# Kernel tuning notes

Measured on AMD Instinct MI355X. Metric: run time of the kernel, lower is better.

The kernel has to match this reference:

```python
import jax, jax.numpy as jnp
import numpy as np

NUM_LAYERS = 4
D_MODEL = 1024
N_HEAD = 8
HEAD_DIM = D_MODEL // N_HEAD
FFN_DIM = 4096
B, L = 8, 512
LN_EPS = 1e-5


def rel_pos_embed(seq_len, dim, init_size=1200, padding_idx=0):
    # RelativeSinusoidalPositionalEmbedding.get_embedding(init_size+1, dim, 0)
    num = init_size + 1  # 1201
    half = dim // 2
    inv = np.exp(np.arange(half, dtype=np.float64) * -(np.log(10000.0) / (half - 1)))
    pos = np.arange(-num // 2, num // 2, dtype=np.float64)[:, None] * inv[None, :]
    emb = np.concatenate([np.sin(pos), np.cos(pos)], axis=1)  # [num, dim]
    emb[padding_idx] = 0.0
    origin_shift = num // 2 + 1  # 601
    idx = np.arange(-seq_len, seq_len) + origin_shift  # [2L]
    return jnp.asarray(emb[idx], dtype=jnp.float32)  # [2L, dim]


def _shift(BD):
    # [b,h,L,2L] -> [b,h,L,L], selecting relative offsets k-q
    b, h, l, _ = BD.shape
    BD = jnp.concatenate([BD, jnp.zeros((b, h, l, 1), BD.dtype)], axis=-1)
    BD = BD.reshape(b, h, -1, l)[:, :, :-1].reshape(b, h, l, 2 * l)
    return BD[:, :, :, l:]


def _transpose_shift(E):
    # [b,h,L,2L] -> [b,h,L,L]
    b, h, l, _ = E.shape
    E = jnp.concatenate([E, jnp.zeros((b, h, l, 1), E.dtype)], axis=-1)
    E = E.reshape(b, h, 2 * l + 1, l)
    E = E[:, :, 2 * jnp.arange(l) + 1, :]  # [b,h,L,L]
    return jnp.swapaxes(E, -1, -2)


def layer_norm(x, g, b):
    mu = x.mean(-1, keepdims=True)
    var = ((x - mu) ** 2).mean(-1, keepdims=True)
    return (x - mu) / jnp.sqrt(var + LN_EPS) * g + b


def rel_attn(x, mask, qkv_w, r_r, r_w, pos):
    bsz, l, d = x.shape
    qkv = x @ qkv_w  # [b,L,3D]
    q, k, v = jnp.split(qkv, 3, axis=-1)
    to_heads = lambda t: t.reshape(bsz, l, N_HEAD, HEAD_DIM).transpose(0, 2, 1, 3)
    q, k, v = to_heads(q), to_heads(k), to_heads(v)  # [b,h,L,hd]
    rw_q = q + r_r[:, None]  # (original adds r_r_bias here)
    AC = jnp.einsum('bnqd,bnkd->bnqk', rw_q, k)
    D_ = jnp.einsum('nd,ld->nl', r_w, pos)[None, :, None]   # [1,h,1,2L]
    B_ = jnp.einsum('bnqd,ld->bnql', q, pos)                # [b,h,L,2L]
    E_ = jnp.einsum('bnqd,ld->bnql', k, pos)
    BDE = _shift(B_ + D_) + _transpose_shift(E_)
    attn = AC + BDE  # scale == 1 (scale=False)
    attn = jnp.where(mask[:, None, None, :] == 0, -jnp.inf, attn)
    attn = jax.nn.softmax(attn, axis=-1)
    out = jnp.einsum('bnqk,bnkd->bnqd', attn, v)
    return out.transpose(0, 2, 1, 3).reshape(bsz, l, d)


def setup_inputs() -> dict:
    key = jax.random.key(0)
    ks = jax.random.split(key, 12)
    Ln = NUM_LAYERS
    s = 0.02
    return {
        'x': jax.random.normal(ks[0], (B, L, D_MODEL), jnp.float32),
        'mask': jnp.ones((B, L), jnp.int32),
        'qkv_w': jax.random.normal(ks[1], (Ln, D_MODEL, 3 * D_MODEL), jnp.float32) * s,
        'r_r_bias': jax.random.normal(ks[2], (Ln, N_HEAD, HEAD_DIM), jnp.float32) * s,
        'r_w_bias': jax.random.normal(ks[3], (Ln, N_HEAD, HEAD_DIM), jnp.float32) * s,
        'ln1_g': jnp.ones((Ln, D_MODEL), jnp.float32),
        'ln1_b': jnp.zeros((Ln, D_MODEL), jnp.float32),
        'ln2_g': jnp.ones((Ln, D_MODEL), jnp.float32),
        'ln2_b': jnp.zeros((Ln, D_MODEL), jnp.float32),
        'w1': jax.random.normal(ks[4], (Ln, D_MODEL, FFN_DIM), jnp.float32) * s,
        'b1': jnp.zeros((Ln, FFN_DIM), jnp.float32),
        'w2': jax.random.normal(ks[5], (Ln, FFN_DIM, D_MODEL), jnp.float32) * s,
        'b2': jnp.zeros((Ln, D_MODEL), jnp.float32),
    }


def reference(x, mask, qkv_w, r_r_bias, r_w_bias, ln1_g, ln1_b, ln2_g, ln2_b, w1, b1, w2, b2):
    pos = rel_pos_embed(x.shape[1], HEAD_DIM)  # [2L, hd], buffer (detached)
    for i in range(NUM_LAYERS):  # after_norm=True (post-LN)
        a = rel_attn(x, mask, qkv_w[i], r_r_bias[i], r_w_bias[i], pos)
        x = layer_norm(x + a, ln1_g[i], ln1_b[i])
        h = jax.nn.relu(x @ w1[i] + b1[i]) @ w2[i] + b2[i]
        x = layer_norm(x + h, ln2_g[i], ln2_b[i])
    return x
```

## Files before the change

kernel.cpp:

```cpp
#include <hip/hip_runtime.h>

#define SEQ 512
#define DM 1024
#define NH 8
#define HD 128
#define FFN 4096
#define NL 4
#define NB 8

typedef __attribute__((ext_vector_type(8))) _Float16 half8v;
typedef __attribute__((ext_vector_type(8))) unsigned short ushort8v;
typedef __attribute__((ext_vector_type(4))) float float4v;

__device__ __forceinline__ unsigned short f2h(float f) {
  _Float16 h = (_Float16)f;
  return *(unsigned short*)&h;
}
__device__ __forceinline__ float h2f(unsigned short u) {
  _Float16 h = *(_Float16*)&u;
  return (float)h;
}

__global__ void prep_kernel(float* __restrict__ sc,
                            const float* __restrict__ in, float* __restrict__ xout,
                            unsigned short* __restrict__ xh) {
  if (blockIdx.x < 128) {
    int idx = blockIdx.x * 256 + threadIdx.x;
    int q = idx >> 6, c = idx & 63;
    double a = exp(-(double)c * (9.210340371976184 / 63.0));
    double p = (double)q * a;
    sc[q * 128 + c] = (float)sin(p);
    sc[q * 128 + 64 + c] = (float)cos(p);
  } else {
    int i = (blockIdx.x - 128) * 256 + threadIdx.x;
    float4 v = ((const float4*)in)[i];
    ((float4*)xout)[i] = v;
    ushort4 u;
    u.x = f2h(v.x); u.y = f2h(v.y); u.z = f2h(v.z); u.w = f2h(v.w);
    ((ushort4*)xh)[i] = u;
  }
}

__global__ __launch_bounds__(256) void transpose_cvt3(
    const float* __restrict__ qw, const float* __restrict__ w1,
    const float* __restrict__ w2,
    unsigned short* __restrict__ wqt, unsigned short* __restrict__ w1t,
    unsigned short* __restrict__ w2t)
{
  __shared__ float t[32][33];
  int id = blockIdx.x;
  const float* in;
  unsigned short* out;
  int K, N, loc;
  if (id < 3072)      { in = qw; out = wqt; K = 1024; N = 3072; loc = id; }
  else if (id < 7168) { in = w1; out = w1t; K = 1024; N = 4096; loc = id - 3072; }
  else                { in = w2; out = w2t; K = 4096; N = 1024; loc = id - 7168; }
  int nx = N >> 5;
  int n0 = (loc % nx) * 32, k0 = (loc / nx) * 32;
  int c = threadIdx.x & 31, r = threadIdx.x >> 5;
#pragma unroll
  for (int i = 0; i < 32; i += 8)
    t[r + i][c] = in[(long long)(k0 + r + i) * N + n0 + c];
  __syncthreads();
#pragma unroll
  for (int i = 0; i < 32; i += 8)
    out[(long long)(n0 + r + i) * K + k0 + c] = f2h(t[c][r + i]);
}

template<int R, int T>
__device__ __forceinline__ void stage_tile(
    const unsigned short* __restrict__ g, long long ld, int k0,
    unsigned short* lds, int tid) {
#pragma unroll
  for (int i = 0; i < R * 64 / 8 / T; i++) {
    int p = i * T + tid;
    int row = p >> 3, cs = p & 7;
    int c = cs ^ (row & 7);
    const unsigned short* src = g + (long long)row * ld + k0 + c * 8;
    __builtin_amdgcn_global_load_lds(
        (const __attribute__((address_space(1))) void*)src,
        (__attribute__((address_space(3))) void*)(lds + p * 8),
        16, 0, 0);
  }
}

__device__ __forceinline__ void load_stage128(
    const unsigned short* __restrict__ g, long long ld, int k0, int tid, ushort8v* v) {
#pragma unroll
  for (int i = 0; i < 2; i++) {
    int p = i * 512 + tid;
    int row = p >> 3, cs = p & 7;
    int c = cs ^ (row & 7);
    v[i] = *(const ushort8v*)(g + (long long)row * ld + k0 + c * 8);
  }
}
__device__ __forceinline__ void write_stage128(
    unsigned short* St, int tid, const ushort8v* v) {
#pragma unroll
  for (int i = 0; i < 2; i++)
    *(ushort8v*)(St + (i * 512 + tid) * 8) = v[i];
}

template<int BIAS, int RELU, int OUTH>
__global__ __launch_bounds__(512, 2) void gemm256(
    const unsigned short* __restrict__ A, int lda, long long sAz,
    const unsigned short* __restrict__ Bt, int ldb, long long sBz,
    const float* __restrict__ bias,
    void* __restrict__ Cv, int ldc, long long sCz,
    int K) {
  __shared__ __align__(16) unsigned short As[2][256 * 64];
  __shared__ __align__(16) unsigned short Bs[2][256 * 64];
  const int tid = threadIdx.x, lane = tid & 63, w = tid >> 6;
  const int wm = w >> 2, wn = w & 3;
  const int l15 = lane & 15, l4 = lane >> 4;
  const int gx = gridDim.x, gy = gridDim.y;
  int nwg = gx * gy * gridDim.z;
  int lin = (blockIdx.z * gy + blockIdx.y) * gx + blockIdx.x;
  int swz = (lin & 7) * (nwg >> 3) + (lin >> 3);
  int bx = swz % gx;
  int t2 = swz / gx;
  int by = t2 % gy;
  int z  = t2 / gy;
  const unsigned short* Ag = A + (long long)z * sAz + (long long)by * 256 * lda;
  const unsigned short* Bg = Bt + (long long)z * sBz + (long long)bx * 256 * ldb;

  float4v acc[8][4] = {};
  const int nt = K >> 6;
  stage_tile<256, 512>(Ag, lda, 0, As[0], tid);
  stage_tile<256, 512>(Bg, ldb, 0, Bs[0], tid);
  int cur = 0;
  for (int t = 0; t < nt; t++) {
    if (t + 1 < nt) {
      stage_tile<256, 512>(Ag, lda, (t + 1) << 6, As[cur ^ 1], tid);
      stage_tile<256, 512>(Bg, ldb, (t + 1) << 6, Bs[cur ^ 1], tid);
      asm volatile("s_waitcnt vmcnt(8)" ::: "memory");
    } else {
      asm volatile("s_waitcnt vmcnt(0)" ::: "memory");
    }
    asm volatile("s_barrier" ::: "memory");
#pragma unroll
    for (int ks = 0; ks < 2; ks++) {
      half8v af[8], bf[4];
#pragma unroll
      for (int m = 0; m < 8; m++) {
        int row = wm * 128 + m * 16 + l15;
        int cs = (ks * 4 + l4) ^ (row & 7);
        af[m] = *(const half8v*)&As[cur][row * 64 + cs * 8];
      }
#pragma unroll
      for (int n = 0; n < 4; n++) {
        int row = wn * 64 + n * 16 + l15;
        int cs = (ks * 4 + l4) ^ (row & 7);
        bf[n] = *(const half8v*)&Bs[cur][row * 64 + cs * 8];
      }
#pragma unroll
      for (int m = 0; m < 8; m++)
#pragma unroll
        for (int n = 0; n < 4; n++)
          acc[m][n] = __builtin_amdgcn_mfma_f32_16x16x32_f16(af[m], bf[n], acc[m][n], 0, 0, 0);
    }
    asm volatile("s_barrier" ::: "memory");
    cur ^= 1;
  }
#pragma unroll
  for (int n = 0; n < 4; n++) {
    int ccol = bx * 256 + wn * 64 + n * 16 + l15;
    float bv = BIAS ? bias[ccol] : 0.f;
#pragma unroll
    for (int m = 0; m < 8; m++) {
      int crow0 = by * 256 + wm * 128 + m * 16 + l4 * 4;
#pragma unroll
      for (int j = 0; j < 4; j++) {
        float v = acc[m][n][j] + bv;
        if (RELU) v = fmaxf(v, 0.f);
        long long off = (long long)z * sCz + (long long)(crow0 + j) * ldc + ccol;
        if (OUTH) ((unsigned short*)Cv)[off] = f2h(v);
        else      ((float*)Cv)[off] = v;
      }
    }
  }
}

__global__ __launch_bounds__(256) void build_attn(
    const unsigned short* __restrict__ qkv_h,
    const float* __restrict__ rr, const float* __restrict__ rw,
    const float* __restrict__ sc,
    unsigned short* __restrict__ Ahat, unsigned short* __restrict__ Bhat,
    unsigned short* __restrict__ Vt)
{
  const int z = blockIdx.y, b = z >> 3, h = z & 7;
  if (blockIdx.x < 256) {
    const int r = threadIdx.x >> 7, lane = threadIdx.x & 127;
    const int q = blockIdx.x * 2 + r;
    __shared__ float Qf[2][128], Kf[2][128], SC[2][128];
    const unsigned short* row = qkv_h + ((long long)(b * SEQ + q)) * 3072 + h * HD;
    float qv = h2f(row[lane]);
    float kv = h2f(row[DM + lane]);
    Qf[r][lane] = qv + rw[h * HD + lane];
    Kf[r][lane] = kv;
    SC[r][lane] = sc[q * 128 + lane];
    __syncthreads();
    unsigned short* Arow = Ahat + ((long long)z * SEQ + q) * 384;
    unsigned short* Brow = Bhat + ((long long)z * SEQ + q) * 384;
    Arow[lane] = f2h(qv + rr[h * HD + lane]);
    Brow[lane] = f2h(kv);
    if (lane < 64) {
      float S = SC[r][lane], C = SC[r][64 + lane];
      Arow[128 + lane] = f2h(Qf[r][lane] * C + Qf[r][64 + lane] * S);
      Arow[256 + lane] = f2h(S);
      Brow[128 + lane] = f2h(S);
      Brow[256 + lane] = f2h(Kf[r][lane] * C + Kf[r][64 + lane] * S);
    } else {
      int c = lane - 64;
      float S = SC[r][c], C = SC[r][lane];
      Arow[192 + c] = f2h(Qf[r][lane] * C - Qf[r][c] * S);
      Arow[320 + c] = f2h(C);
      Brow[192 + c] = f2h(C);
      Brow[320 + c] = f2h(Kf[r][lane] * C - Kf[r][c] * S);
    }
  } else {
    __shared__ unsigned short t[32][33];
    int tile = blockIdx.x - 256;
    const int d0 = (tile & 3) * 32, j0 = (tile >> 2) * 32;
    const int c = threadIdx.x & 31, r = threadIdx.x >> 5;
#pragma unroll
    for (int i = 0; i < 32; i += 8)
      t[r + i][c] = qkv_h[((long long)(b * SEQ + j0 + r + i)) * 3072 + 2 * DM + h * HD + d0 + c];
    __syncthreads();
#pragma unroll
    for (int i = 0; i < 32; i += 8)
      Vt[(long long)z * HD * SEQ + (long long)(d0 + r + i) * SEQ + j0 + c] = t[c][r + i];
  }
}

__global__ __launch_bounds__(512, 4) void attn_fused(
    const unsigned short* __restrict__ Ahat,
    const unsigned short* __restrict__ Bhat,
    const unsigned short* __restrict__ Vt,
    const int* __restrict__ mask,
    unsigned short* __restrict__ out)
{
  __shared__ __align__(16) unsigned short S[64 * 512];
  __shared__ __align__(16) unsigned short St[128 * 64];
  const int tid = threadIdx.x, lane = tid & 63, w = tid >> 6;
  const int wr = w >> 1, wc = w & 1;
  const int l15 = lane & 15, l4 = lane >> 4;
  int lin = blockIdx.z * gridDim.x + blockIdx.x;
  int nwg = gridDim.x * gridDim.z;
  int swz = (lin & 7) * (nwg >> 3) + (lin >> 3);
  int qt = swz % gridDim.x, z = swz / gridDim.x;
  const int b = z >> 3, h = z & 7;
  const int q0 = qt * 64;

  half8v qf[12];
  {
    const unsigned short* Ar = Ahat + ((long long)z * SEQ + q0 + wr * 16 + l15) * 384;
#pragma unroll
    for (int k = 0; k < 12; k++)
      qf[k] = *(const half8v*)&Ar[k * 32 + l4 * 8];
  }

  ushort8v stg[2];
  load_stage128(Bhat + ((long long)z * SEQ) * 384, 384, 0, tid, stg);
#pragma unroll
  for (int jt = 0; jt < 4; jt++) {
    float4v acc[4] = {};
#pragma unroll
    for (int k6 = 0; k6 < 6; k6++) {
      __builtin_amdgcn_s_barrier();
      write_stage128(St, tid, stg);
      int ns = jt * 6 + k6 + 1;
      if (ns < 24) {
        const unsigned short* Bg = Bhat + ((long long)z * SEQ + (ns / 6) * 128) * 384;
        load_stage128(Bg, 384, (ns % 6) * 64, tid, stg);
      }
      asm volatile("s_waitcnt lgkmcnt(0)" ::: "memory");
      __builtin_amdgcn_s_barrier();
      __builtin_amdgcn_s_setprio(1);
#pragma unroll
      for (int kk = 0; kk < 2; kk++) {
        int kidx = k6 * 2 + kk;
#pragma unroll
        for (int n = 0; n < 4; n++) {
          int row = wc * 64 + n * 16 + l15;
          int cs = (kk * 4 + l4) ^ (row & 7);
          half8v bf = *(const half8v*)&St[row * 64 + cs * 8];
          acc[n] = __builtin_amdgcn_mfma_f32_16x16x32_f16(qf[kidx], bf, acc[n], 0, 0, 0);
        }
      }
      __builtin_amdgcn_s_setprio(0);
    }
#pragma unroll
    for (int n = 0; n < 4; n++) {
      int col = jt * 128 + wc * 64 + n * 16 + l15;
#pragma unroll
      for (int j = 0; j < 4; j++) {
        int row = wr * 16 + l4 * 4 + j;
        int byte = (row * 512 + col) * 2;
        byte ^= (row & 7) << 4;
        *(unsigned short*)((char*)S + byte) = f2h(acc[n][j]);
      }
    }
  }

  const unsigned short* Vg = Vt + (long long)z * HD * SEQ;
  load_stage128(Vg, 512, 0, tid, stg);

  asm volatile("s_waitcnt lgkmcnt(0)" ::: "memory");
  __builtin_amdgcn_s_barrier();

  float* bias = (float*)St;
  float* Linv = (float*)St + 512;
  if (tid < 128) {
    int4 mk = ((const int4*)(mask + (size_t)b * SEQ))[tid];
    float4 bv;
    bv.x = mk.x ? 0.f : -1e30f;
    bv.y = mk.y ? 0.f : -1e30f;
    bv.z = mk.z ? 0.f : -1e30f;
    bv.w = mk.w ? 0.f : -1e30f;
    ((float4*)bias)[tid] = bv;
  }
  asm volatile("s_waitcnt lgkmcnt(0)" ::: "memory");
  __builtin_amdgcn_s_barrier();
  {
    const int row = tid >> 3;
    const int c8 = tid & 7;
    float mx = -1e30f;
#pragma unroll
    for (int i = 0; i < 8; i++) {
      int col = i * 64 + c8 * 8;
      int byte = (row * 512 + col) * 2;
      byte ^= (row & 7) << 4;
      ushort8v u = *(const ushort8v*)((const char*)S + byte);
      const float* bp = bias + col;
#pragma unroll
      for (int e = 0; e < 8; e++)
        mx = fmaxf(mx, h2f(u[e]) + bp[e]);
    }
    mx = fmaxf(mx, __shfl_xor(mx, 1));
    mx = fmaxf(mx, __shfl_xor(mx, 2));
    mx = fmaxf(mx, __shfl_xor(mx, 4));
    float sum = 0.f;
#pragma unroll
    for (int i = 0; i < 8; i++) {
      int col = i * 64 + c8 * 8;
      int byte = (row * 512 + col) * 2;
      byte ^= (row & 7) << 4;
      ushort8v u = *(const ushort8v*)((const char*)S + byte);
      const float* bp = bias + col;
#pragma unroll
      for (int e = 0; e < 8; e++) {
        float ev = __expf(h2f(u[e]) + bp[e] - mx);
        sum += ev;
        u[e] = f2h(ev);
      }
      *(ushort8v*)((char*)S + byte) = u;
    }
    sum += __shfl_xor(sum, 1);
    sum += __shfl_xor(sum, 2);
    sum += __shfl_xor(sum, 4);
    if (c8 == 0) Linv[row] = 1.f / sum;
  }
  asm volatile("s_waitcnt lgkmcnt(0)" ::: "memory");
  __builtin_amdgcn_s_barrier();
  float rs[4];
#pragma unroll
  for (int j = 0; j < 4; j++) rs[j] = Linv[wr * 16 + l4 * 4 + j];
  asm volatile("s_waitcnt lgkmcnt(0)" ::: "memory");

  float4v oacc[4] = {};
#pragma unroll
  for (int k8 = 0; k8 < 8; k8++) {
    __builtin_amdgcn_s_barrier();
    write_stage128(St, tid, stg);
    if (k8 + 1 < 8) load_stage128(Vg, 512, (k8 + 1) * 64, tid, stg);
    asm volatile("s_waitcnt lgkmcnt(0)" ::: "memory");
    __builtin_amdgcn_s_barrier();
    __builtin_amdgcn_s_setprio(1);
#pragma unroll
    for (int kk = 0; kk < 2; kk++) {
      int prow = wr * 16 + l15;
      int pb = (prow * 512 + k8 * 64 + kk * 32 + l4 * 8) * 2;
      pb ^= (prow & 7) << 4;
      half8v af = *(const half8v*)((const char*)S + pb);
#pragma unroll
      for (int n = 0; n < 4; n++) {
        int row = wc * 64 + n * 16 + l15;
        int cs = (kk * 4 + l4) ^ (row & 7);
        half8v bf = *(const half8v*)&St[row * 64 + cs * 8];
        oacc[n] = __builtin_amdgcn_mfma_f32_16x16x32_f16(af, bf, oacc[n], 0, 0, 0);
      }
    }
    __builtin_amdgcn_s_setprio(0);
  }
#pragma unroll
  for (int j = 0; j < 4; j++) {
    int row = q0 + wr * 16 + l4 * 4 + j;
#pragma unroll
    for (int n = 0; n < 4; n++) {
      int col = h * HD + wc * 64 + n * 16 + l15;
      out[((long long)(b * SEQ + row)) * DM + col] = f2h(oacc[n][j] * rs[j]);
    }
  }
}

__global__ __launch_bounds__(256) void add_ln_cvt(
    float* __restrict__ x, const unsigned short* __restrict__ a,
    const float* __restrict__ g, const float* __restrict__ bt,
    unsigned short* __restrict__ xh)
{
  const int row = blockIdx.x, tid = threadIdx.x;
  float4* xp = (float4*)(x + (size_t)row * DM);
  const ushort4 av = ((const ushort4*)(a + (size_t)row * DM))[tid];
  float4 xv = xp[tid];
  float4 s = make_float4(xv.x + h2f(av.x), xv.y + h2f(av.y),
                         xv.z + h2f(av.z), xv.w + h2f(av.w));
  __shared__ float red[4];
  float sum = s.x + s.y + s.z + s.w;
  for (int o = 32; o; o >>= 1) sum += __shfl_down(sum, o);
  if ((tid & 63) == 0) red[tid >> 6] = sum;
  __syncthreads();
  float mu = (red[0] + red[1] + red[2] + red[3]) * (1.f / DM);
  float dx = s.x - mu, dy = s.y - mu, dz = s.z - mu, dw = s.w - mu;
  float sq = dx * dx + dy * dy + dz * dz + dw * dw;
  for (int o = 32; o; o >>= 1) sq += __shfl_down(sq, o);
  __syncthreads();
  if ((tid & 63) == 0) red[tid >> 6] = sq;
  __syncthreads();
  float var = (red[0] + red[1] + red[2] + red[3]) * (1.f / DM);
  float rstd = rsqrtf(var + 1e-5f);
  const float4 gv = ((const float4*)g)[tid];
  const float4 bv = ((const float4*)bt)[tid];
  float4 o4 = make_float4(dx * rstd * gv.x + bv.x, dy * rstd * gv.y + bv.y,
                          dz * rstd * gv.z + bv.z, dw * rstd * gv.w + bv.w);
  xp[tid] = o4;
  ushort4 u;
  u.x = f2h(o4.x); u.y = f2h(o4.y); u.z = f2h(o4.z); u.w = f2h(o4.w);
  ((ushort4*)(xh + (size_t)row * DM))[tid] = u;
}

__global__ __launch_bounds__(256) void add_ln_cvt4(
    float* __restrict__ x, const unsigned short* __restrict__ p, long long pstride,
    const float* __restrict__ bias,
    const float* __restrict__ g, const float* __restrict__ bt,
    unsigned short* __restrict__ xh)
{
  const int row = blockIdx.x, tid = threadIdx.x;
  float4* xp = (float4*)(x + (size_t)row * DM);
  const float4 bb = ((const float4*)bias)[tid];
  float4 xv = xp[tid];
  float4 s = make_float4(xv.x + bb.x, xv.y + bb.y, xv.z + bb.z, xv.w + bb.w);
#pragma unroll
  for (int zz = 0; zz < 4; zz++) {
    const ushort4 a = ((const ushort4*)(p + zz * pstride + (size_t)row * DM))[tid];
    s.x += h2f(a.x); s.y += h2f(a.y); s.z += h2f(a.z); s.w += h2f(a.w);
  }
  __shared__ float red[4];
  float sum = s.x + s.y + s.z + s.w;
  for (int o = 32; o; o >>= 1) sum += __shfl_down(sum, o);
  if ((tid & 63) == 0) red[tid >> 6] = sum;
  __syncthreads();
  float mu = (red[0] + red[1] + red[2] + red[3]) * (1.f / DM);
  float dx = s.x - mu, dy = s.y - mu, dz = s.z - mu, dw = s.w - mu;
  float sq = dx * dx + dy * dy + dz * dz + dw * dw;
  for (int o = 32; o; o >>= 1) sq += __shfl_down(sq, o);
  __syncthreads();
  if ((tid & 63) == 0) red[tid >> 6] = sq;
  __syncthreads();
  float var = (red[0] + red[1] + red[2] + red[3]) * (1.f / DM);
  float rstd = rsqrtf(var + 1e-5f);
  const float4 gv = ((const float4*)g)[tid];
  const float4 bv = ((const float4*)bt)[tid];
  float4 o4 = make_float4(dx * rstd * gv.x + bv.x, dy * rstd * gv.y + bv.y,
                          dz * rstd * gv.z + bv.z, dw * rstd * gv.w + bv.w);
  xp[tid] = o4;
  ushort4 u;
  u.x = f2h(o4.x); u.y = f2h(o4.y); u.z = f2h(o4.z); u.w = f2h(o4.w);
  ((ushort4*)(xh + (size_t)row * DM))[tid] = u;
}

extern "C" void kernel_launch(void* const* d_in, const int* in_sizes, int n_in,
                              void* d_out, int out_size, void* d_ws, size_t ws_size,
                              hipStream_t stream)
{
  const float* x_in = (const float*)d_in[0];
  const int*   mask = (const int*)d_in[1];
  const float* qkv_w = (const float*)d_in[2];
  const float* r_r  = (const float*)d_in[3];
  const float* r_w  = (const float*)d_in[4];
  const float* ln1g = (const float*)d_in[5];
  const float* ln1b = (const float*)d_in[6];
  const float* ln2g = (const float*)d_in[7];
  const float* ln2b = (const float*)d_in[8];
  const float* w1   = (const float*)d_in[9];
  const float* b1   = (const float*)d_in[10];
  const float* w2   = (const float*)d_in[11];
  const float* b2   = (const float*)d_in[12];
  float* x = (float*)d_out;
  char* ws = (char*)d_ws;

  const int ROWS = NB * SEQ;

  const size_t sc_off   = 0;
  const size_t xh_off   = 0x40000;
  const size_t wqt_off  = xh_off + (size_t)ROWS * DM * 2;
  const size_t w1t_off  = wqt_off + (size_t)3 * DM * DM * 2;
  const size_t w2t_off  = w1t_off + (size_t)FFN * DM * 2;
  const size_t a16_off  = w2t_off + (size_t)FFN * DM * 2;
  const size_t qkvh_off = a16_off + (size_t)ROWS * DM * 2;
  const size_t e_off    = qkvh_off + (size_t)ROWS * 3 * DM * 2;

  const size_t ab_bytes = (size_t)64 * SEQ * 384 * 2;
  const size_t hb_bytes = (size_t)ROWS * FFN * 2;
  const size_t part_off = e_off + hb_bytes;

  float* sc     = (float*)(ws + sc_off);
  unsigned short* xh = (unsigned short*)(ws + xh_off);
  unsigned short* wqt = (unsigned short*)(ws + wqt_off);
  unsigned short* w1t = (unsigned short*)(ws + w1t_off);
  unsigned short* w2t = (unsigned short*)(ws + w2t_off);
  unsigned short* a16 = (unsigned short*)(ws + a16_off);
  unsigned short* qkvh = (unsigned short*)(ws + qkvh_off);
  unsigned short* Ahat = (unsigned short*)(ws + e_off);
  unsigned short* Bhat = (unsigned short*)(ws + e_off + ab_bytes);
  unsigned short* Vt   = (unsigned short*)(ws + e_off + 2 * ab_bytes);
  unsigned short* hb = (unsigned short*)(ws + e_off);
  unsigned short* part = (unsigned short*)(ws + part_off);

  prep_kernel<<<dim3(128 + ROWS * DM / 4 / 256), 256, 0, stream>>>(sc, x_in, x, xh);

  for (int L = 0; L < NL; L++) {
    transpose_cvt3<<<dim3(11264), 256, 0, stream>>>(
        qkv_w + (size_t)L * DM * 3 * DM, w1 + (size_t)L * DM * FFN,
        w2 + (size_t)L * FFN * DM, wqt, w1t, w2t);

    gemm256<0,0,1><<<dim3(3 * DM / 256, ROWS / 256, 1), 512, 0, stream>>>(
        xh, DM, 0, wqt, DM, 0, nullptr, qkvh, 3 * DM, 0, DM);

    build_attn<<<dim3(256 + 64, 64), 256, 0, stream>>>(
        qkvh, r_r + (size_t)L * NH * HD, r_w + (size_t)L * NH * HD, sc, Ahat, Bhat, Vt);
    attn_fused<<<dim3(SEQ / 64, 1, 64), 512, 0, stream>>>(Ahat, Bhat, Vt, mask, a16);

    add_ln_cvt<<<dim3(ROWS), 256, 0, stream>>>(x, a16, ln1g + (size_t)L * DM, ln1b + (size_t)L * DM, xh);

    gemm256<1,1,1><<<dim3(FFN / 256, ROWS / 256, 1), 512, 0, stream>>>(
        xh, DM, 0, w1t, DM, 0, b1 + (size_t)L * FFN, hb, FFN, 0, DM);

    gemm256<0,0,1><<<dim3(DM / 256, ROWS / 256, 4), 512, 0, stream>>>(
        hb, FFN, 1024, w2t, FFN, 1024, nullptr,
        part, DM, (long long)ROWS * DM, 1024);

    add_ln_cvt4<<<dim3(ROWS), 256, 0, stream>>>(
        x, part, (long long)ROWS * DM, b2 + (size_t)L * DM,
        ln2g + (size_t)L * DM, ln2b + (size_t)L * DM, xh);
  }
}
```

Before: 838.4 us.

## Split GEMM K-tile into half-stages with finer-grained interleaved prefetch and setprio

Restructures the 256x256 GEMM main loop so each 64-wide K tile is split into two 32-wide LDS sub-buffers. Global-to-LDS loads are issued in small chunks between four MFMA phases, with barriers between phases and s_setprio raised around the MFMA blocks, in the style of ping-pong scheduling. The goal is to overlap memory traffic with matrix math more evenly and to cut LDS bank conflicts through a new XOR swizzle. The cost is many more barriers per iteration and delicate vmcnt accounting that could stall or race if any count is wrong.

```diff
diff --git a/kernel.cpp b/kernel.cpp
--- a/kernel.cpp
+++ b/kernel.cpp
@@ -84,6 +84,22 @@
   }
 }
 
+__device__ __forceinline__ void stageK(
+    const unsigned short* __restrict__ g, long long ld, int k0,
+    unsigned short* lds, int tid) {
+#pragma unroll
+  for (int i = 0; i < 2; i++) {
+    int p = i * 512 + tid;
+    int row = p >> 2, cs = p & 3;
+    int c = cs ^ ((row >> 1) & 3);
+    const unsigned short* src = g + (long long)row * ld + k0 + c * 8;
+    __builtin_amdgcn_global_load_lds(
+        (const __attribute__((address_space(1))) void*)src,
+        (__attribute__((address_space(3))) void*)(lds + p * 8),
+        16, 0, 0);
+  }
+}
+
 __device__ __forceinline__ void load_stage128(
     const unsigned short* __restrict__ g, long long ld, int k0, int tid, ushort8v* v) {
 #pragma unroll
@@ -108,8 +124,8 @@
     const float* __restrict__ bias,
     void* __restrict__ Cv, int ldc, long long sCz,
     int K) {
-  __shared__ __align__(16) unsigned short As[2][256 * 64];
-  __shared__ __align__(16) unsigned short Bs[2][256 * 64];
+  __shared__ __align__(16) unsigned short As[2][2][256 * 32];
+  __shared__ __align__(16) unsigned short Bs[2][2][256 * 32];
   const int tid = threadIdx.x, lane = tid & 63, w = tid >> 6;
   const int wm = w >> 2, wn = w & 3;
   const int l15 = lane & 15, l4 = lane >> 4;
@@ -126,41 +142,91 @@
 
   float4v acc[8][4] = {};
   const int nt = K >> 6;
-  stage_tile<256, 512>(Ag, lda, 0, As[0], tid);
-  stage_tile<256, 512>(Bg, ldb, 0, Bs[0], tid);
-  int cur = 0;
+  stageK(Ag, lda, 0,  As[0][0], tid); stageK(Bg, ldb, 0,  Bs[0][0], tid);
+  stageK(Ag, lda, 32, As[0][1], tid); stageK(Bg, ldb, 32, Bs[0][1], tid);
+  stageK(Ag, lda, 64, As[1][0], tid); stageK(Bg, ldb, 64, Bs[1][0], tid);
+  stageK(Ag, lda, 96, As[1][1], tid);
+  asm volatile("s_waitcnt vmcnt(6)" ::: "memory");
+  asm volatile("s_barrier" ::: "memory");
+
+  half8v af[8], bf[4];
   for (int t = 0; t < nt; t++) {
-    if (t + 1 < nt) {
-      stage_tile<256, 512>(Ag, lda, (t + 1) << 6, As[cur ^ 1], tid);
-      stage_tile<256, 512>(Bg, ldb, (t + 1) << 6, Bs[cur ^ 1], tid);
-      asm volatile("s_waitcnt vmcnt(8)" ::: "memory");
+    const int cur = t & 1, nxt = cur ^ 1;
+#pragma unroll
+    for (int m = 0; m < 8; m++) {
+      int row = wm * 128 + m * 16 + l15;
+      af[m] = *(const half8v*)&As[cur][0][row * 32 + (l4 ^ ((row >> 1) & 3)) * 8];
+    }
+#pragma unroll
+    for (int n = 0; n < 2; n++) {
+      int row = wn * 64 + n * 16 + l15;
+      bf[n] = *(const half8v*)&Bs[cur][0][row * 32 + (l4 ^ ((row >> 1) & 3)) * 8];
+    }
+    if (t + 1 < nt) stageK(Bg, ldb, ((t + 1) << 6) + 32, Bs[nxt][1], tid);
+    asm volatile("s_barrier" ::: "memory");
+    __builtin_amdgcn_s_setprio(1);
+#pragma unroll
+    for (int m = 0; m < 8; m++)
+#pragma unroll
+      for (int n = 0; n < 2; n++)
+        acc[m][n] = __builtin_amdgcn_mfma_f32_16x16x32_f16(af[m], bf[n], acc[m][n], 0, 0, 0);
+    __builtin_amdgcn_s_setprio(0);
+    asm volatile("s_barrier" ::: "memory");
+#pragma unroll
+    for (int n = 0; n < 2; n++) {
+      int row = wn * 64 + (2 + n) * 16 + l15;
+      bf[2 + n] = *(const half8v*)&Bs[cur][0][row * 32 + (l4 ^ ((row >> 1) & 3)) * 8];
+    }
+    if (t + 2 < nt) stageK(Ag, lda, (t + 2) << 6, As[cur][0], tid);
+    asm volatile("s_barrier" ::: "memory");
+    __builtin_amdgcn_s_setprio(1);
+#pragma unroll
+    for (int m = 0; m < 8; m++)
+#pragma unroll
+      for (int n = 0; n < 2; n++)
+        acc[m][2 + n] = __builtin_amdgcn_mfma_f32_16x16x32_f16(af[m], bf[2 + n], acc[m][2 + n], 0, 0, 0);
+    __builtin_amdgcn_s_setprio(0);
+    asm volatile("s_barrier" ::: "memory");
+#pragma unroll
+    for (int m = 0; m < 8; m++) {
+      int row = wm * 128 + m * 16 + l15;
+      af[m] = *(const half8v*)&As[cur][1][row * 32 + (l4 ^ ((row >> 1) & 3)) * 8];
+    }
+#pragma unroll
+    for (int n = 0; n < 2; n++) {
+      int row = wn * 64 + n * 16 + l15;
+      bf[n] = *(const half8v*)&Bs[cur][1][row * 32 + (l4 ^ ((row >> 1) & 3)) * 8];
+    }
+    if (t + 2 < nt) stageK(Bg, ldb, (t + 2) << 6, Bs[cur][0], tid);
+    asm volatile("s_barrier" ::: "memory");
+    __builtin_amdgcn_s_setprio(1);
+#pragma unroll
+    for (int m = 0; m < 8; m++)
+#pragma unroll
+      for (int n = 0; n < 2; n++)
+        acc[m][n] = __builtin_amdgcn_mfma_f32_16x16x32_f16(af[m], bf[n], acc[m][n], 0, 0, 0);
+    __builtin_amdgcn_s_setprio(0);
+    asm volatile("s_barrier" ::: "memory");
+#pragma unroll
+    for (int n = 0; n < 2; n++) {
+      int row = wn * 64 + (2 + n) * 16 + l15;
+      bf[2 + n] = *(const half8v*)&Bs[cur][1][row * 32 + (l4 ^ ((row >> 1) & 3)) * 8];
+    }
+    if (t + 2 < nt) {
+      stageK(Ag, lda, ((t + 2) << 6) + 32, As[cur][1], tid);
+      asm volatile("s_waitcnt vmcnt(6)" ::: "memory");
     } else {
       asm volatile("s_waitcnt vmcnt(0)" ::: "memory");
     }
     asm volatile("s_barrier" ::: "memory");
-#pragma unroll
-    for (int ks = 0; ks < 2; ks++) {
-      half8v af[8], bf[4];
-#pragma unroll
-      for (int m = 0; m < 8; m++) {
-        int row = wm * 128 + m * 16 + l15;
-        int cs = (ks * 4 + l4) ^ (row & 7);
-        af[m] = *(const half8v*)&As[cur][row * 64 + cs * 8];
-      }
-#pragma unroll
-      for (int n = 0; n < 4; n++) {
-        int row = wn * 64 + n * 16 + l15;
-        int cs = (ks * 4 + l4) ^ (row & 7);
-        bf[n] = *(const half8v*)&Bs[cur][row * 64 + cs * 8];
-      }
-#pragma unroll
-      for (int m = 0; m < 8; m++)
-#pragma unroll
-        for (int n = 0; n < 4; n++)
-          acc[m][n] = __builtin_amdgcn_mfma_f32_16x16x32_f16(af[m], bf[n], acc[m][n], 0, 0, 0);
-    }
-    asm volatile("s_barrier" ::: "memory");
-    cur ^= 1;
+    __builtin_amdgcn_s_setprio(1);
+#pragma unroll
+    for (int m = 0; m < 8; m++)
+#pragma unroll
+      for (int n = 0; n < 2; n++)
+        acc[m][2 + n] = __builtin_amdgcn_mfma_f32_16x16x32_f16(af[m], bf[2 + n], acc[m][2 + n], 0, 0, 0);
+    __builtin_amdgcn_s_setprio(0);
+    asm volatile("s_barrier" ::: "memory");
   }
 #pragma unroll
   for (int n = 0; n < 4; n++) {
```

After: 829.4 us, median of 2. Within noise of the previous version (-1.1%).
